# Optimization experiments

Measured on AMD Instinct MI355X. Metric: run time of the kernel, lower is better.

Reference implementation:

```python
import jax, jax.numpy as jnp
import numpy as np

B, S, E, H = 1, 2048, 4096, 32
D = E // H
MAX_POS = 2048
NEG_MASK = -66504.0
SCALE = float(np.sqrt(D))


def _rope(x, position_ids):
    # x: [B, S, H, D]; GPT-NeoX style rotate-half rotary embedding
    half = D // 2
    inv_freq = 1.0 / (10000.0 ** (jnp.arange(0, half, dtype=jnp.float32) * 2.0 / D))  # [D/2]
    ang = position_ids.astype(jnp.float32)[:, None] * inv_freq[None, :]               # [S, D/2]
    cos = jnp.cos(ang)[None, :, None, :]
    sin = jnp.sin(ang)[None, :, None, :]
    x1, x2 = x[..., :half], x[..., half:]
    return jnp.concatenate([x1 * cos - x2 * sin, x2 * cos + x1 * sin], axis=-1)


def setup_inputs() -> dict:
    key = jax.random.key(0)
    ks = jax.random.split(key, 9)
    s = 0.02
    return {
        "hidden_states": jax.random.normal(ks[0], (B, S, E), jnp.float32),
        "wq": jax.random.normal(ks[1], (E, E), jnp.float32) * s,
        "bq": jnp.zeros((E,), jnp.float32),
        "wk": jax.random.normal(ks[2], (E, E), jnp.float32) * s,
        "bk": jnp.zeros((E,), jnp.float32),
        "wv": jax.random.normal(ks[3], (E, E), jnp.float32) * s,
        "bv": jnp.zeros((E,), jnp.float32),
        "wo": jax.random.normal(ks[4], (E, E), jnp.float32) * s,
        "bo": jnp.zeros((E,), jnp.float32),
        "position_ids": jnp.arange(S, dtype=jnp.int32),
    }


def reference(hidden_states, wq, bq, wk, bk, wv, bv, wo, bo, position_ids):
    # QKV projections (nn.Linear: x @ W.T + b)
    q = hidden_states @ wq.T + bq
    k = hidden_states @ wk.T + bk
    v = hidden_states @ wv.T + bv
    # [B, S, H, D]
    q = q.reshape(B, S, H, D)
    k = k.reshape(B, S, H, D)
    v = v.reshape(B, S, H, D)
    # rotary embedding on key and query
    q = _rope(q, position_ids)
    k = _rope(k, position_ids)
    # [B, H, S, D]
    q = q.transpose(0, 2, 1, 3)
    k = k.transpose(0, 2, 1, 3)
    v = v.transpose(0, 2, 1, 3)
    # attention scores; causal mask added BEFORE dividing by scale (faithful to source)
    scores = jnp.einsum("bhqd,bhkd->bhqk", q, k)
    causal = (1.0 - jnp.tril(jnp.ones((S, S), jnp.float32))) * NEG_MASK  # [S, S]
    scores = (scores + causal[None, None]) / SCALE
    attn = jax.nn.softmax(scores.astype(jnp.float32), axis=-1).astype(q.dtype)
    ctx = jnp.einsum("bhqk,bhkd->bhqd", attn, v)
    ctx = ctx.transpose(0, 2, 1, 3).reshape(B, S, E)
    return ctx @ wo.T + bo
```

## Files before the change

kernel.cpp:

```cpp
#include <hip/hip_runtime.h>
#include <hip/hip_bf16.h>

constexpr int SEQ = 2048;
constexpr int EMB = 4096;
constexpr int NH  = 32;
constexpr int HD  = 128;
constexpr int HALF = 64;

typedef __bf16 bf16x8 __attribute__((ext_vector_type(8)));
typedef float  f32x4  __attribute__((ext_vector_type(4)));
using u16 = unsigned short;
typedef u16 ushort8 __attribute__((ext_vector_type(8)));
typedef u16 u16x4 __attribute__((ext_vector_type(4)));

__device__ inline float bf2f(u16 u) {
  union { unsigned int i; float f; } v; v.i = ((unsigned int)u) << 16; return v.f;
}
__device__ inline u16 f2bf(float f) {
  union { __bf16 b; u16 u; } v; v.b = (__bf16)f; return v.u;
}

#define GLL16(gp, lp) __builtin_amdgcn_global_load_lds( \
    (const __attribute__((address_space(1))) void*)(gp), \
    (__attribute__((address_space(3))) void*)(lp), 16, 0, 0)

__global__ void k_f32_to_bf16(const float* __restrict__ in, u16* __restrict__ out, int n) {
  int i = (blockIdx.x * blockDim.x + threadIdx.x) * 8;
  if (i >= n) return;
  f32x4 a = *(const f32x4*)(in + i);
  f32x4 b = *(const f32x4*)(in + i + 4);
  ushort8 o;
  o[0] = f2bf(a[0]); o[1] = f2bf(a[1]); o[2] = f2bf(a[2]); o[3] = f2bf(a[3]);
  o[4] = f2bf(b[0]); o[5] = f2bf(b[1]); o[6] = f2bf(b[2]); o[7] = f2bf(b[3]);
  *(ushort8*)(out + i) = o;
}

__global__ void k_rope_table(const int* __restrict__ pos, float* __restrict__ tab) {
  int idx = blockIdx.x * blockDim.x + threadIdx.x;
  if (idx >= SEQ * HALF) return;
  int s = idx >> 6, d = idx & 63;
  double invf = pow(10000.0, -(double)d / 64.0);
  double ang = (double)pos[s] * invf;
  tab[idx * 2]     = (float)cos(ang);
  tab[idx * 2 + 1] = (float)sin(ang);
}

__global__ void k_rope(u16* __restrict__ X, const float* __restrict__ tab, float scale) {
  int idx = blockIdx.x * blockDim.x + threadIdx.x;
  if (idx >= SEQ * NH * HALF) return;
  int d = idx & 63;
  int h = (idx >> 6) & 31;
  int s = idx >> 11;
  u16* p = X + (size_t)s * EMB + h * HD + d;
  float x1 = bf2f(p[0]), x2 = bf2f(p[HALF]);
  float c  = tab[(s * HALF + d) * 2];
  float sn = tab[(s * HALF + d) * 2 + 1];
  p[0]    = f2bf((x1 * c - x2 * sn) * scale);
  p[HALF] = f2bf((x2 * c + x1 * sn) * scale);
}

__global__ __launch_bounds__(512) void k_gemm8(
    const u16* __restrict__ Ag, const u16* __restrict__ Wg,
    const float* __restrict__ b0, const float* __restrict__ b1, const float* __restrict__ b2,
    void* __restrict__ C0, void* __restrict__ C1, void* __restrict__ C2,
    int M, int N, int K, int mode)
{
  __shared__ alignas(16) u16 As[3][128 * 64];
  __shared__ alignas(16) u16 Bs[3][256 * 64];

  int tid = threadIdx.x;
  int lane = tid & 63, wid = tid >> 6;
  int wm = wid >> 2, wn = wid & 3;
  int l15 = lane & 15, lhi = lane >> 4;

  int NBY = M / 128, NBX = N / 256;
  int wg = blockIdx.x;
  int xcd = wg & 7, sgl = wg >> 3;
  int by = sgl % NBY, bxl = sgl / NBY;
  int bx = xcd * (NBX >> 3) + bxl;
  int m0 = by * 128, n0 = bx * 256;

  auto stageA = [&](int b, int k0) {
#pragma unroll
    for (int s2 = 0; s2 < 2; s2++) {
      int row = s2 * 64 + (tid >> 3);
      int kb = ((tid & 7) - row) & 7;
      GLL16(Ag + (size_t)(m0 + row) * K + k0 + kb * 8, &As[b][s2 * 4096 + tid * 8]);
    }
  };
  auto stageBh = [&](int b, int k0, int h) {
#pragma unroll
    for (int s2 = 0; s2 < 2; s2++) {
      int row = h * 128 + s2 * 64 + (tid >> 3);
      int kb = ((tid & 7) - row) & 7;
      GLL16(Wg + (size_t)(n0 + row) * K + k0 + kb * 8, &Bs[b][h * 8192 + s2 * 4096 + tid * 8]);
    }
  };

  f32x4 acc[4][4] = {};
  int KT = K >> 6;

  stageA(0, 0);  stageBh(0, 0, 0);  stageBh(0, 0, 1);
  stageA(1, 64); stageBh(1, 64, 0); stageBh(1, 64, 1);

  for (int t = 0; t < KT; t++) {
    if (t + 1 < KT) asm volatile("s_waitcnt vmcnt(6)" ::: "memory");
    else            asm volatile("s_waitcnt vmcnt(0)" ::: "memory");
    __builtin_amdgcn_s_barrier();

    const u16* as = &As[t % 3][0];
    const u16* bs = &Bs[t % 3][0];
    bool do_stage = (t + 2) < KT;
    int bstage = (t + 2) % 3;
    int ks = (t + 2) << 6;

    bf16x8 bfr[4][2];
#pragma unroll
    for (int p = 0; p < 4; p++) {
      if (p == 0) {
#pragma unroll
        for (int q = 0; q < 4; q++)
#pragma unroll
          for (int kk = 0; kk < 2; kk++) {
            int row = wn * 64 + q * 16 + l15;
            int pb = (kk * 4 + lhi + row) & 7;
            bfr[q][kk] = *(const bf16x8*)&bs[row * 64 + pb * 8];
          }
      }
      bf16x8 af[2];
#pragma unroll
      for (int kk = 0; kk < 2; kk++) {
        int row = wm * 64 + p * 16 + l15;
        int pb = (kk * 4 + lhi + row) & 7;
        af[kk] = *(const bf16x8*)&as[row * 64 + pb * 8];
      }
      if (do_stage) {
        if (p == 0)      stageA(bstage, ks);
        else if (p == 1) stageBh(bstage, ks, 0);
        else if (p == 2) stageBh(bstage, ks, 1);
      }
      __builtin_amdgcn_s_setprio(1);
#pragma unroll
      for (int q = 0; q < 4; q++)
#pragma unroll
        for (int kk = 0; kk < 2; kk++)
          acc[p][q] = __builtin_amdgcn_mfma_f32_16x16x32_bf16(af[kk], bfr[q][kk], acc[p][q], 0, 0, 0);
      __builtin_amdgcn_s_setprio(0);
    }
  }

  const float* bias = b0;
  void* Cout = C0;
  int mode_l = mode, Nn = N, n_base = n0;
  if (mode == 3) {
    int seg = n0 >> 12;
    Nn = EMB; n_base = n0 & 4095;
    if (seg == 0)      { bias = b0; Cout = C0; mode_l = 0; }
    else if (seg == 1) { bias = b1; Cout = C1; mode_l = 0; }
    else               { bias = b2; Cout = C2; mode_l = 2; }
  }

#pragma unroll
  for (int p = 0; p < 4; p++) {
    int m = m0 + wm * 64 + p * 16 + lhi * 4;
#pragma unroll
    for (int q = 0; q < 4; q++) {
      int n = n_base + wn * 64 + q * 16 + l15;
      float bs2 = bias[n];
      if (mode_l == 2) {
        u16x4 pk;
#pragma unroll
        for (int r = 0; r < 4; r++) pk[r] = f2bf(acc[p][q][r] + bs2);
        *(u16x4*)&((u16*)Cout)[(size_t)n * M + m] = pk;
      } else if (mode_l == 1) {
#pragma unroll
        for (int r = 0; r < 4; r++)
          ((float*)Cout)[(size_t)(m + r) * Nn + n] = acc[p][q][r] + bs2;
      } else {
#pragma unroll
        for (int r = 0; r < 4; r++)
          ((u16*)Cout)[(size_t)(m + r) * Nn + n] = f2bf(acc[p][q][r] + bs2);
      }
    }
  }
}

constexpr int QB = 64, KVB = 64;

__global__ __launch_bounds__(256) void k_flash(
    const u16* __restrict__ Q, const u16* __restrict__ K, const u16* __restrict__ VT,
    u16* __restrict__ ctx)
{
  __shared__ alignas(16) u16 Ks[2][KVB * 128];
  __shared__ alignas(16) u16 Vt[2][HD * 64];
  __shared__ alignas(16) u16 Pl[4][16 * 64];

  int tid = threadIdx.x, lane = tid & 63, wid = tid >> 6;
  int l15 = lane & 15, lhi = lane >> 4;
  int h = blockIdx.y;

  auto stage = [&](int buf, int t2) {
    int kv = t2 * KVB;
#pragma unroll
    for (int it = 0; it < 4; it++) {
      int chunk = tid + it * 256;
      int r = chunk >> 4, bp = chunk & 15;
      GLL16(K + (size_t)(kv + r) * EMB + h * HD + (((bp - r) & 15) << 3), &Ks[buf][chunk * 8]);
    }
#pragma unroll
    for (int it = 0; it < 4; it++) {
      int chunk = tid + it * 256;
      int d = chunk >> 3, bp = chunk & 7;
      GLL16(VT + (size_t)(h * HD + d) * SEQ + kv + (((bp - d) & 7) << 3), &Vt[buf][chunk * 8]);
    }
  };

  for (int pi = 0; pi < 2; pi++) {
    int qb = pi ? (int)blockIdx.x : 31 - (int)blockIdx.x;
    int q0 = qb * QB;
    int qw = q0 + wid * 16;

    bf16x8 qf[4];
#pragma unroll
    for (int kc = 0; kc < 4; kc++)
      qf[kc] = *(const bf16x8*)&Q[(size_t)(qw + l15) * EMB + h * HD + kc * 32 + lhi * 8];

    f32x4 O[8] = {};
    float mrow[4], lrow[4];
#pragma unroll
    for (int r = 0; r < 4; r++) { mrow[r] = -3.0e38f; lrow[r] = 0.f; }

    int nt = qb + 1;
    __syncthreads();
    stage(0, 0);
    for (int t = 0; t < nt; t++) {
      __syncthreads();
      if (t + 1 < nt) stage((t + 1) & 1, t + 1);

      const u16* ks = Ks[t & 1];
      const u16* vt = Vt[t & 1];
      float p[4][4];
      bool need_mask = (t == nt - 1);
#pragma unroll
      for (int c = 0; c < 4; c++) {
        f32x4 s = {};
        int r0 = c * 16 + l15;
#pragma unroll
        for (int kc = 0; kc < 4; kc++) {
          bf16x8 kf = *(const bf16x8*)&ks[r0 * 128 + (((kc * 4 + lhi) + r0) & 15) * 8];
          s = __builtin_amdgcn_mfma_f32_16x16x32_bf16(qf[kc], kf, s, 0, 0, 0);
        }
#pragma unroll
        for (int r = 0; r < 4; r++) {
          float sv = s[r];
          if (need_mask) {
            int qg = qw + lhi * 4 + r;
            int kg = t * KVB + c * 16 + l15;
            if (kg > qg) sv = -3.0e38f;
          }
          p[c][r] = sv;
        }
      }
      float fscale[4];
#pragma unroll
      for (int r = 0; r < 4; r++) {
        float m = fmaxf(fmaxf(p[0][r], p[1][r]), fmaxf(p[2][r], p[3][r]));
#pragma unroll
        for (int x = 1; x < 16; x <<= 1) m = fmaxf(m, __shfl_xor(m, x, 64));
        float mnew = fmaxf(mrow[r], m);
        fscale[r] = __expf(mrow[r] - mnew);
        mrow[r] = mnew;
      }
#pragma unroll
      for (int c = 0; c < 4; c++)
#pragma unroll
        for (int r = 0; r < 4; r++)
          p[c][r] = __expf(p[c][r] - mrow[r]);
#pragma unroll
      for (int r = 0; r < 4; r++) {
        float s = p[0][r] + p[1][r] + p[2][r] + p[3][r];
#pragma unroll
        for (int x = 1; x < 16; x <<= 1) s += __shfl_xor(s, x, 64);
        lrow[r] = lrow[r] * fscale[r] + s;
      }
#pragma unroll
      for (int d = 0; d < 8; d++)
#pragma unroll
        for (int r = 0; r < 4; r++)
          O[d][r] *= fscale[r];
#pragma unroll
      for (int c = 0; c < 4; c++) {
        int kb = c * 2 + (l15 >> 3), klo = l15 & 7;
#pragma unroll
        for (int r = 0; r < 4; r++) {
          int q = lhi * 4 + r;
          Pl[wid][q * 64 + ((kb + (q >> 1)) & 7) * 8 + klo] = f2bf(p[c][r]);
        }
      }
#pragma unroll
      for (int ks2 = 0; ks2 < 2; ks2++) {
        int kb = ks2 * 4 + lhi;
        bf16x8 pf = *(const bf16x8*)&Pl[wid][l15 * 64 + ((kb + (l15 >> 1)) & 7) * 8];
#pragma unroll
        for (int ds = 0; ds < 8; ds++) {
          int d = ds * 16 + l15;
          bf16x8 vf = *(const bf16x8*)&vt[d * 64 + ((kb + d) & 7) * 8];
          O[ds] = __builtin_amdgcn_mfma_f32_16x16x32_bf16(pf, vf, O[ds], 0, 0, 0);
        }
      }
    }

#pragma unroll
    for (int r = 0; r < 4; r++) {
      float inv = 1.f / lrow[r];
      int qg = q0 + wid * 16 + lhi * 4 + r;
#pragma unroll
      for (int ds = 0; ds < 8; ds++)
        ctx[(size_t)qg * EMB + h * HD + ds * 16 + l15] = f2bf(O[ds][r] * inv);
    }
  }
}

extern "C" void kernel_launch(void* const* d_in, const int* in_sizes, int n_in,
                              void* d_out, int out_size, void* d_ws, size_t ws_size,
                              hipStream_t stream) {
  const float* hs = (const float*)d_in[0];
  const float* wq = (const float*)d_in[1];
  const float* bq = (const float*)d_in[2];
  const float* wk = (const float*)d_in[3];
  const float* bk = (const float*)d_in[4];
  const float* wv = (const float*)d_in[5];
  const float* bv = (const float*)d_in[6];
  const float* wo = (const float*)d_in[7];
  const float* bo = (const float*)d_in[8];
  const int*  pos = (const int*)d_in[9];

  const size_t SE = (size_t)SEQ * EMB;
  const size_t EE = (size_t)EMB * EMB;
  const float qscale = 1.0f / 11.313708498984761f;

  char* ws = (char*)d_ws;
  size_t off = 0;
  auto alloc = [&](size_t b) { size_t o = off; off += (b + 255) & ~(size_t)255; return o; };

  size_t need_fused = ((SE * 2 + 255) & ~255ULL) + ((EE * 6 + 255) & ~255ULL) +
                      3 * ((SE * 2 + 255) & ~255ULL) + ((size_t)SEQ * HALF * 8 + 255);
  bool fused = ws_size >= need_fused + 4096;

  u16*  hsb = (u16*)(ws + alloc(SE * 2));
  u16*  wb  = (u16*)(ws + alloc(fused ? EE * 6 : EE * 2));
  u16*  Qb  = (u16*)(ws + alloc(SE * 2));
  u16*  Kb  = (u16*)(ws + alloc(SE * 2));
  u16*  VTb = (u16*)(ws + alloc(SE * 2));
  float* tab = (float*)(ws + alloc((size_t)SEQ * HALF * 2 * 4));
  u16*  ctxb = hsb;

  dim3 cb(256);
  k_f32_to_bf16<<<dim3(SE / 2048), cb, 0, stream>>>(hs, hsb, (int)SE);
  k_rope_table<<<dim3(SEQ * HALF / 256), cb, 0, stream>>>(pos, tab);

  if (fused) {
    k_f32_to_bf16<<<dim3(EE / 2048), cb, 0, stream>>>(wq, wb, (int)EE);
    k_f32_to_bf16<<<dim3(EE / 2048), cb, 0, stream>>>(wk, wb + EE, (int)EE);
    k_f32_to_bf16<<<dim3(EE / 2048), cb, 0, stream>>>(wv, wb + 2 * EE, (int)EE);
    k_gemm8<<<dim3(768), dim3(512), 0, stream>>>(
        hsb, wb, bq, bk, bv, (void*)Qb, (void*)Kb, (void*)VTb, SEQ, 3 * EMB, EMB, 3);
  } else {
    k_f32_to_bf16<<<dim3(EE / 2048), cb, 0, stream>>>(wq, wb, (int)EE);
    k_gemm8<<<dim3(256), dim3(512), 0, stream>>>(
        hsb, wb, bq, bq, bq, (void*)Qb, nullptr, nullptr, SEQ, EMB, EMB, 0);
    k_f32_to_bf16<<<dim3(EE / 2048), cb, 0, stream>>>(wk, wb, (int)EE);
    k_gemm8<<<dim3(256), dim3(512), 0, stream>>>(
        hsb, wb, bk, bk, bk, (void*)Kb, nullptr, nullptr, SEQ, EMB, EMB, 0);
    k_f32_to_bf16<<<dim3(EE / 2048), cb, 0, stream>>>(wv, wb, (int)EE);
    k_gemm8<<<dim3(256), dim3(512), 0, stream>>>(
        hsb, wb, bv, bv, bv, (void*)VTb, nullptr, nullptr, SEQ, EMB, EMB, 2);
  }

  k_rope<<<dim3(SEQ * NH * HALF / 256), cb, 0, stream>>>(Qb, tab, qscale);
  k_rope<<<dim3(SEQ * NH * HALF / 256), cb, 0, stream>>>(Kb, tab, 1.0f);

  k_flash<<<dim3(16, NH), cb, 0, stream>>>(Qb, Kb, VTb, ctxb);

  k_f32_to_bf16<<<dim3(EE / 2048), cb, 0, stream>>>(wo, wb, (int)EE);
  k_gemm8<<<dim3(256), dim3(512), 0, stream>>>(
      ctxb, wb, bo, bo, bo, d_out, nullptr, nullptr, SEQ, EMB, EMB, 1);
}
```

Before: 581.4 us.

## Replace GEMM with templated BK=32 double-buffered kernel and larger M tiles

Rewrites the bf16 GEMM as a template over the M tile size. The K step drops from 64 to 32, the triple buffer becomes a double buffer with a new 4-way LDS swizzle, and all fragment loads now finish before the MFMAs, with extra barriers. The QKV projections use 256x256 tiles, which halves the grid, while the output projection keeps 128x256. It also requests 2 blocks per CU through launch bounds. The aim is more data reuse per tile and higher occupancy, at the risk of a shallower prefetch, more barriers per K step, and fewer blocks available to fill the GPU.

```diff
diff --git a/kernel.cpp b/kernel.cpp
--- a/kernel.cpp
+++ b/kernel.cpp
@@ -59,99 +59,93 @@
   p[HALF] = f2bf((x2 * c + x1 * sn) * scale);
 }
 
-__global__ __launch_bounds__(512) void k_gemm8(
+template<int TBM>
+__global__ __launch_bounds__(512, 2) void k_gemm3(
     const u16* __restrict__ Ag, const u16* __restrict__ Wg,
     const float* __restrict__ b0, const float* __restrict__ b1, const float* __restrict__ b2,
     void* __restrict__ C0, void* __restrict__ C1, void* __restrict__ C2,
     int M, int N, int K, int mode)
 {
-  __shared__ alignas(16) u16 As[3][128 * 64];
-  __shared__ alignas(16) u16 Bs[3][256 * 64];
+  constexpr int MA  = TBM / 32;
+  constexpr int LDA = TBM / 128;
+  constexpr int LPT = LDA + 2;
+  __shared__ alignas(16) u16 As[2][TBM * 32];
+  __shared__ alignas(16) u16 Bs[2][256 * 32];
 
   int tid = threadIdx.x;
   int lane = tid & 63, wid = tid >> 6;
   int wm = wid >> 2, wn = wid & 3;
   int l15 = lane & 15, lhi = lane >> 4;
 
-  int NBY = M / 128, NBX = N / 256;
+  int NBY = M / TBM, NBX = N >> 8;
   int wg = blockIdx.x;
   int xcd = wg & 7, sgl = wg >> 3;
   int by = sgl % NBY, bxl = sgl / NBY;
   int bx = xcd * (NBX >> 3) + bxl;
-  int m0 = by * 128, n0 = bx * 256;
+  int m0 = by * TBM, n0 = bx * 256;
 
   auto stageA = [&](int b, int k0) {
 #pragma unroll
-    for (int s2 = 0; s2 < 2; s2++) {
-      int row = s2 * 64 + (tid >> 3);
-      int kb = ((tid & 7) - row) & 7;
-      GLL16(Ag + (size_t)(m0 + row) * K + k0 + kb * 8, &As[b][s2 * 4096 + tid * 8]);
+    for (int ld = 0; ld < LDA; ld++) {
+      int idx = ld * 512 + tid;
+      int row = idx >> 2, pb = idx & 3;
+      int kb = (pb - row - (row >> 2)) & 3;
+      GLL16(Ag + (size_t)(m0 + row) * K + k0 + kb * 8, &As[b][idx * 8]);
     }
   };
-  auto stageBh = [&](int b, int k0, int h) {
-#pragma unroll
-    for (int s2 = 0; s2 < 2; s2++) {
-      int row = h * 128 + s2 * 64 + (tid >> 3);
-      int kb = ((tid & 7) - row) & 7;
-      GLL16(Wg + (size_t)(n0 + row) * K + k0 + kb * 8, &Bs[b][h * 8192 + s2 * 4096 + tid * 8]);
+  auto stageB = [&](int b, int k0) {
+#pragma unroll
+    for (int ld = 0; ld < 2; ld++) {
+      int idx = ld * 512 + tid;
+      int row = idx >> 2, pb = idx & 3;
+      int kb = (pb - row - (row >> 2)) & 3;
+      GLL16(Wg + (size_t)(n0 + row) * K + k0 + kb * 8, &Bs[b][idx * 8]);
     }
   };
 
-  f32x4 acc[4][4] = {};
-  int KT = K >> 6;
-
-  stageA(0, 0);  stageBh(0, 0, 0);  stageBh(0, 0, 1);
-  stageA(1, 64); stageBh(1, 64, 0); stageBh(1, 64, 1);
-
+  f32x4 acc[MA][4] = {};
+  int KT = K >> 5;
+
+  stageA(0, 0); stageB(0, 0);
   for (int t = 0; t < KT; t++) {
-    if (t + 1 < KT) asm volatile("s_waitcnt vmcnt(6)" ::: "memory");
-    else            asm volatile("s_waitcnt vmcnt(0)" ::: "memory");
+    if (t + 1 < KT) {
+      int nb = (t + 1) & 1, nk = (t + 1) << 5;
+      stageA(nb, nk); stageB(nb, nk);
+      asm volatile("s_waitcnt vmcnt(%0)" :: "n"(LPT) : "memory");
+    } else {
+      asm volatile("s_waitcnt vmcnt(0)" ::: "memory");
+    }
     __builtin_amdgcn_s_barrier();
-
-    const u16* as = &As[t % 3][0];
-    const u16* bs = &Bs[t % 3][0];
-    bool do_stage = (t + 2) < KT;
-    int bstage = (t + 2) % 3;
-    int ks = (t + 2) << 6;
-
-    bf16x8 bfr[4][2];
-#pragma unroll
-    for (int p = 0; p < 4; p++) {
-      if (p == 0) {
-#pragma unroll
-        for (int q = 0; q < 4; q++)
-#pragma unroll
-          for (int kk = 0; kk < 2; kk++) {
-            int row = wn * 64 + q * 16 + l15;
-            int pb = (kk * 4 + lhi + row) & 7;
-            bfr[q][kk] = *(const bf16x8*)&bs[row * 64 + pb * 8];
-          }
-      }
-      bf16x8 af[2];
-#pragma unroll
-      for (int kk = 0; kk < 2; kk++) {
-        int row = wm * 64 + p * 16 + l15;
-        int pb = (kk * 4 + lhi + row) & 7;
-        af[kk] = *(const bf16x8*)&as[row * 64 + pb * 8];
-      }
-      if (do_stage) {
-        if (p == 0)      stageA(bstage, ks);
-        else if (p == 1) stageBh(bstage, ks, 0);
-        else if (p == 2) stageBh(bstage, ks, 1);
-      }
-      __builtin_amdgcn_s_setprio(1);
+    __builtin_amdgcn_sched_barrier(0);
+
+    const u16* as = &As[t & 1][0];
+    const u16* bs = &Bs[t & 1][0];
+    bf16x8 af[MA], bfr[4];
+#pragma unroll
+    for (int q = 0; q < 4; q++) {
+      int row = wn * 64 + q * 16 + l15;
+      bfr[q] = *(const bf16x8*)&bs[row * 32 + ((lhi + row + (row >> 2)) & 3) * 8];
+    }
+#pragma unroll
+    for (int p = 0; p < MA; p++) {
+      int row = wm * (TBM / 2) + p * 16 + l15;
+      af[p] = *(const bf16x8*)&as[row * 32 + ((lhi + row + (row >> 2)) & 3) * 8];
+    }
+    asm volatile("s_waitcnt lgkmcnt(0)" ::: "memory");
+    __builtin_amdgcn_sched_barrier(0);
+    __builtin_amdgcn_s_setprio(1);
+#pragma unroll
+    for (int p = 0; p < MA; p++)
 #pragma unroll
       for (int q = 0; q < 4; q++)
-#pragma unroll
-        for (int kk = 0; kk < 2; kk++)
-          acc[p][q] = __builtin_amdgcn_mfma_f32_16x16x32_bf16(af[kk], bfr[q][kk], acc[p][q], 0, 0, 0);
-      __builtin_amdgcn_s_setprio(0);
-    }
-  }
-
+        acc[p][q] = __builtin_amdgcn_mfma_f32_16x16x32_bf16(af[p], bfr[q], acc[p][q], 0, 0, 0);
+    __builtin_amdgcn_s_setprio(0);
+    __builtin_amdgcn_s_barrier();
+  }
+
+  int mode_l = mode, Nn = N, n_base = n0;
   const float* bias = b0;
   void* Cout = C0;
-  int mode_l = mode, Nn = N, n_base = n0;
   if (mode == 3) {
     int seg = n0 >> 12;
     Nn = EMB; n_base = n0 & 4095;
@@ -161,8 +155,8 @@
   }
 
 #pragma unroll
-  for (int p = 0; p < 4; p++) {
-    int m = m0 + wm * 64 + p * 16 + lhi * 4;
+  for (int p = 0; p < MA; p++) {
+    int m = m0 + wm * (TBM / 2) + p * 16 + lhi * 4;
 #pragma unroll
     for (int q = 0; q < 4; q++) {
       int n = n_base + wn * 64 + q * 16 + l15;
@@ -363,17 +357,17 @@
     k_f32_to_bf16<<<dim3(EE / 2048), cb, 0, stream>>>(wq, wb, (int)EE);
     k_f32_to_bf16<<<dim3(EE / 2048), cb, 0, stream>>>(wk, wb + EE, (int)EE);
     k_f32_to_bf16<<<dim3(EE / 2048), cb, 0, stream>>>(wv, wb + 2 * EE, (int)EE);
-    k_gemm8<<<dim3(768), dim3(512), 0, stream>>>(
+    k_gemm3<256><<<dim3(384), dim3(512), 0, stream>>>(
         hsb, wb, bq, bk, bv, (void*)Qb, (void*)Kb, (void*)VTb, SEQ, 3 * EMB, EMB, 3);
   } else {
     k_f32_to_bf16<<<dim3(EE / 2048), cb, 0, stream>>>(wq, wb, (int)EE);
-    k_gemm8<<<dim3(256), dim3(512), 0, stream>>>(
+    k_gemm3<256><<<dim3(128), dim3(512), 0, stream>>>(
         hsb, wb, bq, bq, bq, (void*)Qb, nullptr, nullptr, SEQ, EMB, EMB, 0);
     k_f32_to_bf16<<<dim3(EE / 2048), cb, 0, stream>>>(wk, wb, (int)EE);
-    k_gemm8<<<dim3(256), dim3(512), 0, stream>>>(
+    k_gemm3<256><<<dim3(128), dim3(512), 0, stream>>>(
         hsb, wb, bk, bk, bk, (void*)Kb, nullptr, nullptr, SEQ, EMB, EMB, 0);
     k_f32_to_bf16<<<dim3(EE / 2048), cb, 0, stream>>>(wv, wb, (int)EE);
-    k_gemm8<<<dim3(256), dim3(512), 0, stream>>>(
+    k_gemm3<256><<<dim3(128), dim3(512), 0, stream>>>(
         hsb, wb, bv, bv, bv, (void*)VTb, nullptr, nullptr, SEQ, EMB, EMB, 2);
   }
 
@@ -383,6 +377,6 @@
   k_flash<<<dim3(16, NH), cb, 0, stream>>>(Qb, Kb, VTb, ctxb);
 
   k_f32_to_bf16<<<dim3(EE / 2048), cb, 0, stream>>>(wo, wb, (int)EE);
-  k_gemm8<<<dim3(256), dim3(512), 0, stream>>>(
+  k_gemm3<128><<<dim3(256), dim3(512), 0, stream>>>(
       ctxb, wb, bo, bo, bo, d_out, nullptr, nullptr, SEQ, EMB, EMB, 1);
 }
```

Result: slower. 626.3 us (+7.7%).
